# Optimization experiments

Hardware: AMD Instinct MI355X
Metric: run time of the kernel (lower is better)

## Reference

```python
import jax, jax.numpy as jnp
import numpy as np

V, E, H, C, T = 100000, 300, 512, 40, 4096  # vocab, embed, hidden, num_classes, seq_len


def setup_inputs() -> dict:
    key = jax.random.key(0)
    ks = jax.random.split(key, 19)
    s = lambda k, shape: jax.random.normal(k, shape, jnp.float32) * 0.05
    inp = {"x": jax.random.randint(ks[0], (T,), 0, V, dtype=jnp.int32)}
    inp["emb"] = s(ks[1], (V, E))  # frozen embedding table
    # PyTorch LSTM params, gate order (i, f, g, o); layer0 in=E, layer1 in=2H
    inp["Wih0f"] = s(ks[2], (4 * H, E)); inp["Whh0f"] = s(ks[3], (4 * H, H)); inp["b0f"] = s(ks[4], (4 * H,))
    inp["Wih0b"] = s(ks[5], (4 * H, E)); inp["Whh0b"] = s(ks[6], (4 * H, H)); inp["b0b"] = s(ks[7], (4 * H,))
    inp["Wih1f"] = s(ks[8], (4 * H, 2 * H)); inp["Whh1f"] = s(ks[9], (4 * H, H)); inp["b1f"] = s(ks[10], (4 * H,))
    inp["Wih1b"] = s(ks[11], (4 * H, 2 * H)); inp["Whh1b"] = s(ks[12], (4 * H, H)); inp["b1b"] = s(ks[13], (4 * H,))
    inp["Wc"] = s(ks[14], (C, 2 * H)); inp["bc"] = s(ks[15], (C,))
    inp["trans"] = s(ks[16], (C, C))  # CRF transitions prev->next
    inp["start"] = s(ks[17], (C,)); inp["end"] = s(ks[18], (C,))
    return inp


def _lstm_dir(x, Wih, Whh, b, reverse):
    # x: (T, D) unbatched; returns hidden states (T, H)
    Hd = Whh.shape[1]
    def step(carry, xt):
        h, c = carry
        g = xt @ Wih.T + h @ Whh.T + b  # (4H,)
        i, f, gg, o = jnp.split(g, 4)
        i = jax.nn.sigmoid(i); f = jax.nn.sigmoid(f)
        gg = jnp.tanh(gg); o = jax.nn.sigmoid(o)
        c = f * c + i * gg
        h = o * jnp.tanh(c)
        return (h, c), h
    xs = x[::-1] if reverse else x
    init = (jnp.zeros((Hd,), x.dtype), jnp.zeros((Hd,), x.dtype))
    _, hs = jax.lax.scan(step, init, xs)
    return hs[::-1] if reverse else hs


def _viterbi(emissions, trans, start, end):
    # emissions: (T, C); returns best path (T,) int32
    def fwd(score, em):
        m = score[:, None] + trans  # (C_prev, C_next)
        bp = jnp.argmax(m, axis=0).astype(jnp.int32)
        return jnp.max(m, axis=0) + em, bp
    score0 = start + emissions[0]
    final, bps = jax.lax.scan(fwd, score0, emissions[1:])  # bps: (T-1, C)
    last = jnp.argmax(final + end).astype(jnp.int32)
    def back(tag, bp):
        prev = bp[tag]
        return prev, prev
    _, path = jax.lax.scan(back, last, bps, reverse=True)  # tags 0..T-2 in order
    return jnp.concatenate([path, last[None]])


def reference(x, emb, Wih0f, Whh0f, b0f, Wih0b, Whh0b, b0b, Wih1f, Whh1f, b1f, Wih1b, Whh1b, b1b, Wc, bc, trans, start, end):
    e = emb[x]  # (T, E); dropout is identity at eval
    h0 = jnp.concatenate([_lstm_dir(e, Wih0f, Whh0f, b0f, False),
                          _lstm_dir(e, Wih0b, Whh0b, b0b, True)], axis=-1)  # (T, 2H)
    h1 = jnp.concatenate([_lstm_dir(h0, Wih1f, Whh1f, b1f, False),
                          _lstm_dir(h0, Wih1b, Whh1b, b1b, True)], axis=-1)  # (T, 2H)
    o = h1 @ Wc.T + bc  # (T, C)
    tag_scores = jax.nn.log_softmax(o, axis=1)
    tags = _viterbi(tag_scores, trans, start, end)
    return tag_scores, tags
```

## Files before the change

kernel.cpp:

```cpp
#include <hip/hip_runtime.h>


typedef unsigned int u32;
typedef unsigned long long u64;
typedef u32 u32x4 __attribute__((ext_vector_type(4)));

#define TT 4096
#define HH 512
#define CC 40
#define NG 2048

__device__ __forceinline__ float sigm(float x) { return 1.0f / (1.0f + __expf(-x)); }
__device__ __forceinline__ float tanh_(float x) { return 1.0f - 2.0f / (__expf(2.0f * x) + 1.0f); }

__device__ __forceinline__ void st_sys_u32(u32* p, u32 v) {
    asm volatile("global_store_dword %0, %1, off sc0 sc1"
                 :
                 : "v"(p), "v"(v)
                 : "memory");
}

__device__ __forceinline__ void ld_mall_b256(const float* p, u32x4& r0, u32x4& r1) {
    asm volatile(
        "global_load_dwordx4 %0, %2, off sc0 sc1\n\t"
        "global_load_dwordx4 %1, %2, off offset:16 sc0 sc1\n\t"
        "s_waitcnt vmcnt(0)"
        : "=&v"(r0), "=&v"(r1)
        : "v"(p)
        : "memory");
}

__global__ __launch_bounds__(256, 2) void gemm_f32_k(const float* __restrict__ A0,
                                                     const float* __restrict__ A1,
                                                     const int* __restrict__ xidx,
                                                     const float* __restrict__ W,
                                                     const float* __restrict__ bias,
                                                     float* __restrict__ C,
                                                     int M, int N, int K, int Ksplit) {
    __shared__ float sA[8][132];
    __shared__ float sW[8][132];
    int tid = threadIdx.x;
    int bn = blockIdx.x, bm = blockIdx.y;
    int tx = tid & 15, ty = tid >> 4;
    int srow = tid >> 1, skh = (tid & 1) * 4;

    int am = bm * 128 + srow;
    const float* arow0;
    const float* arow1 = nullptr;
    if (xidx) {
        arow0 = A0 + (size_t)xidx[am] * K;
    } else {
        arow0 = A0 + (size_t)am * Ksplit;
        arow1 = A1 + (size_t)am * Ksplit;
    }
    const float* wrow = W + (size_t)(bn * 128 + srow) * K;

    float acc[2][2][4][4] = {};

    for (int kc = 0; kc < K; kc += 8) {
        float4 av, wv;
        int k0 = kc + skh;
        if (kc + 8 <= K) {
            if (xidx || k0 + 4 <= Ksplit) av = *(const float4*)(arow0 + k0);
            else                          av = *(const float4*)(arow1 + (k0 - Ksplit));
            wv = *(const float4*)(wrow + k0);
        } else {
            float a_[4], w_[4];
#pragma unroll
            for (int j = 0; j < 4; j++) {
                int k = k0 + j;
                bool ok = k < K;
                a_[j] = ok ? ((xidx || k < Ksplit) ? arow0[k] : arow1[k - Ksplit]) : 0.f;
                w_[j] = ok ? wrow[k] : 0.f;
            }
            av = make_float4(a_[0], a_[1], a_[2], a_[3]);
            wv = make_float4(w_[0], w_[1], w_[2], w_[3]);
        }
        __syncthreads();
        sA[skh + 0][srow] = av.x; sA[skh + 1][srow] = av.y;
        sA[skh + 2][srow] = av.z; sA[skh + 3][srow] = av.w;
        sW[skh + 0][srow] = wv.x; sW[skh + 1][srow] = wv.y;
        sW[skh + 2][srow] = wv.z; sW[skh + 3][srow] = wv.w;
        __syncthreads();
#pragma unroll
        for (int k = 0; k < 8; k++) {
            float4 a0 = *(const float4*)&sA[k][ty * 4];
            float4 a1 = *(const float4*)&sA[k][64 + ty * 4];
            float4 w0 = *(const float4*)&sW[k][tx * 4];
            float4 w1 = *(const float4*)&sW[k][64 + tx * 4];
            float am_[2][4] = {{a0.x, a0.y, a0.z, a0.w}, {a1.x, a1.y, a1.z, a1.w}};
            float wn_[2][4] = {{w0.x, w0.y, w0.z, w0.w}, {w1.x, w1.y, w1.z, w1.w}};
#pragma unroll
            for (int p = 0; p < 2; p++)
#pragma unroll
                for (int q = 0; q < 2; q++)
#pragma unroll
                    for (int mi = 0; mi < 4; mi++)
#pragma unroll
                        for (int ni = 0; ni < 4; ni++)
                            acc[p][q][mi][ni] += am_[p][mi] * wn_[q][ni];
        }
    }

#pragma unroll
    for (int q = 0; q < 2; q++) {
        int gn = bn * 128 + q * 64 + tx * 4;
        float4 b4 = *(const float4*)&bias[gn];
#pragma unroll
        for (int p = 0; p < 2; p++) {
            int gm = bm * 128 + p * 64 + ty * 4;
#pragma unroll
            for (int mi = 0; mi < 4; mi++) {
                float4 o;
                o.x = acc[p][q][mi][0] + b4.x; o.y = acc[p][q][mi][1] + b4.y;
                o.z = acc[p][q][mi][2] + b4.z; o.w = acc[p][q][mi][3] + b4.w;
                *(float4*)&C[(size_t)(gm + mi) * N + gn] = o;
            }
        }
    }
}

__global__ __attribute__((amdgpu_flat_work_group_size(512, 512), amdgpu_waves_per_eu(2, 2)))
void lstm_phase_k(const float* __restrict__ WxF,
                  const float* __restrict__ WxB,
                  const float* __restrict__ WhhF,
                  const float* __restrict__ WhhB,
                  float* __restrict__ histF,
                  float* __restrict__ histB,
                  int phase) {
    const int wg = blockIdx.x & 31;
    const int dir = blockIdx.x >> 5;
    const int tid = threadIdx.x;
    const float* Wx = dir ? WxB : WxF;
    const float* Whh = dir ? WhhB : WhhF;
    float* hist = dir ? histB : histF;
    const u32 ENC = phase ? 0x7F800000u : 0u;

    const int r = tid >> 3, seg = tid & 7;
    const int grow = (r >> 4) * 512 + wg * 16 + (r & 15);

    float w[64];
    {
        const float* wr = Whh + (size_t)grow * HH + seg * 64;
#pragma unroll
        for (int i = 0; i < 16; i++) {
            float4 v = *(const float4*)(wr + i * 4);
            w[i * 4 + 0] = v.x; w[i * 4 + 1] = v.y; w[i * 4 + 2] = v.z; w[i * 4 + 3] = v.w;
        }
    }

    const int j = (tid < 62) ? (tid + (tid >= wg * 2 ? 2 : 0)) : 0;

    __shared__ float lds_h[8 * 68];
    __shared__ float lds_g[64];
    float c_state = 0.f;
    int capped = 0;

    for (int s = 0; s < TT; ++s) {
        const int t = dir ? (TT - 1 - s) : s;
        float wxv = 0.f;
        if (seg == 0) wxv = Wx[(size_t)t * NG + grow];

        if (s > 0) {
            const int tprev = dir ? (t + 1) : (t - 1);
            if (tid < 62) {
                const float* p = hist + (size_t)tprev * HH + j * 8;
                u32x4 v0, v1;
                if (!capped) {
                    int it = 0;
                    for (;;) {
                        ld_mall_b256(p, v0, v1);
                        bool ok;
                        if (phase) {
                            ok = ((v0.x & 0x7F800000u) >= 0x40000000u) &&
                                 ((v0.y & 0x7F800000u) >= 0x40000000u) &&
                                 ((v0.z & 0x7F800000u) >= 0x40000000u) &&
                                 ((v0.w & 0x7F800000u) >= 0x40000000u) &&
                                 ((v1.x & 0x7F800000u) >= 0x40000000u) &&
                                 ((v1.y & 0x7F800000u) >= 0x40000000u) &&
                                 ((v1.z & 0x7F800000u) >= 0x40000000u) &&
                                 ((v1.w & 0x7F800000u) >= 0x40000000u);
                        } else {
                            ok = (v0.x != 0xAAAAAAAAu) && (v0.y != 0xAAAAAAAAu) &&
                                 (v0.z != 0xAAAAAAAAu) && (v0.w != 0xAAAAAAAAu) &&
                                 (v1.x != 0xAAAAAAAAu) && (v1.y != 0xAAAAAAAAu) &&
                                 (v1.z != 0xAAAAAAAAu) && (v1.w != 0xAAAAAAAAu);
                        }
                        if (ok) break;
                        if (++it > (1 << 18)) { capped = 1; break; }
                    }
                } else {
                    ld_mall_b256(p, v0, v1);
                }
                float* dst = &lds_h[(j >> 3) * 68 + ((j & 7) * 8)];
                float4 f0, f1;
                f0.x = __uint_as_float(v0.x ^ ENC); f0.y = __uint_as_float(v0.y ^ ENC);
                f0.z = __uint_as_float(v0.z ^ ENC); f0.w = __uint_as_float(v0.w ^ ENC);
                f1.x = __uint_as_float(v1.x ^ ENC); f1.y = __uint_as_float(v1.y ^ ENC);
                f1.z = __uint_as_float(v1.z ^ ENC); f1.w = __uint_as_float(v1.w ^ ENC);
                *(float4*)dst = f0;
                *(float4*)(dst + 4) = f1;
            }
            __syncthreads();
            float a0 = 0.f, a1 = 0.f, a2 = 0.f, a3 = 0.f;
            const float4* hv4 = (const float4*)&lds_h[seg * 68];
#pragma unroll
            for (int i = 0; i < 16; i++) {
                float4 hv = hv4[i];
                a0 += w[i * 4 + 0] * hv.x;
                a1 += w[i * 4 + 1] * hv.y;
                a2 += w[i * 4 + 2] * hv.z;
                a3 += w[i * 4 + 3] * hv.w;
            }
            float acc = (a0 + a1) + (a2 + a3);
            acc += __shfl_xor(acc, 1);
            acc += __shfl_xor(acc, 2);
            acc += __shfl_xor(acc, 4);
            if (seg == 0) lds_g[r] = acc + wxv;
        } else {
            if (seg == 0) lds_g[r] = wxv;
        }
        __syncthreads();

        if (tid < 16) {
            float gi = lds_g[tid], gf = lds_g[16 + tid], gg = lds_g[32 + tid], go = lds_g[48 + tid];
            float iv = sigm(gi), fv = sigm(gf), gv = tanh_(gg), ov = sigm(go);
            c_state = fv * c_state + iv * gv;
            float h = ov * tanh_(c_state);
            int hidx = wg * 16 + tid;
            lds_h[(hidx >> 6) * 68 + (hidx & 63)] = h;
            st_sys_u32((u32*)&hist[(size_t)t * HH + hidx], __float_as_uint(h) ^ ENC);
        }
    }
}

__global__ __launch_bounds__(64, 4) void classifier_k(const float* __restrict__ histF,
                                                      const float* __restrict__ histB,
                                                      const float* __restrict__ Wc,
                                                      const float* __restrict__ bc,
                                                      float* __restrict__ outsc) {
    int t = blockIdx.x, lane = threadIdx.x;
    __shared__ float hrow[1024];
    const uint4* hf4 = (const uint4*)(histF + (size_t)t * HH);
    const uint4* hb4 = (const uint4*)(histB + (size_t)t * HH);
#pragma unroll
    for (int jj = 0; jj < 4; jj++) {
        int idx4 = jj * 64 + lane;
        uint4 u = (idx4 < 128) ? hf4[idx4] : hb4[idx4 - 128];
        u.x ^= 0x7F800000u; u.y ^= 0x7F800000u; u.z ^= 0x7F800000u; u.w ^= 0x7F800000u;
        float4 v;
        v.x = __uint_as_float(u.x); v.y = __uint_as_float(u.y);
        v.z = __uint_as_float(u.z); v.w = __uint_as_float(u.w);
        *(float4*)&hrow[idx4 * 4] = v;
    }
    __syncthreads();
    float o = 0.f;
    if (lane < CC) {
        o = bc[lane];
        const float4* wr = (const float4*)(Wc + (size_t)lane * 1024);
#pragma unroll 4
        for (int kk = 0; kk < 256; ++kk) {
            float4 w4 = wr[kk];
            float4 h4 = *(const float4*)&hrow[kk * 4];
            o += w4.x * h4.x + w4.y * h4.y + w4.z * h4.z + w4.w * h4.w;
        }
    }
    float m = (lane < CC) ? o : -1e30f;
#pragma unroll
    for (int d = 1; d < 64; d <<= 1) m = fmaxf(m, __shfl_xor(m, d));
    float ex = (lane < CC) ? __expf(o - m) : 0.f;
#pragma unroll
    for (int d = 1; d < 64; d <<= 1) ex += __shfl_xor(ex, d);
    float lse = m + __logf(ex);
    if (lane < CC) outsc[(size_t)t * CC + lane] = o - lse;
}

__global__ __launch_bounds__(64) void viterbi_k(const float* __restrict__ em,
                                               const float* __restrict__ trans,
                                               const float* __restrict__ startv,
                                               const float* __restrict__ endv,
                                               unsigned char* __restrict__ bp,
                                               float* __restrict__ outtags) {
    int lane = threadIdx.x;
    float tcol[CC];
#pragma unroll
    for (int p = 0; p < CC; p++) tcol[p] = 0.f;
    if (lane < CC) {
#pragma unroll
        for (int p = 0; p < CC; p++) tcol[p] = trans[p * CC + lane];
    }
    float s = (lane < CC) ? (startv[lane] + em[lane]) : 0.f;

    for (int t = 1; t < TT; ++t) {
        float emv = (lane < CC) ? em[(size_t)t * CC + lane] : 0.f;
        float b0 = -1e30f, b1 = -1e30f;
        int i0 = 0, i1 = 20;
#pragma unroll
        for (int p = 0; p < 20; p++) {
            float c0 = __shfl(s, p) + tcol[p];
            float c1 = __shfl(s, p + 20) + tcol[p + 20];
            if (c0 > b0) { b0 = c0; i0 = p; }
            if (c1 > b1) { b1 = c1; i1 = p + 20; }
        }
        float best = b0; int bi = i0;
        if (b1 > b0) { best = b1; bi = i1; }
        s = best + emv;
        if (lane < CC) bp[(size_t)t * CC + lane] = (unsigned char)bi;
    }
    float fv = (lane < CC) ? (s + endv[lane]) : -1e30f;
    int fi = (lane < CC) ? lane : 63;
#pragma unroll
    for (int d = 1; d < 64; d <<= 1) {
        float ov = __shfl_xor(fv, d);
        int oi = __shfl_xor(fi, d);
        if (ov > fv || (ov == fv && oi < fi)) { fv = ov; fi = oi; }
    }
    __threadfence();
    if (lane == 0) {
        int cur = fi;
        outtags[TT - 1] = (float)cur;
        for (int t = TT - 2; t >= 0; --t) {
            cur = bp[(size_t)(t + 1) * CC + cur];
            outtags[t] = (float)cur;
        }
    }
}

extern "C" void kernel_launch(void* const* d_in, const int* in_sizes, int n_in,
                              void* d_out, int out_size, void* d_ws, size_t ws_size,
                              hipStream_t stream) {
    const int*   x     = (const int*)d_in[0];
    const float* emb   = (const float*)d_in[1];
    const float* Wih0f = (const float*)d_in[2];
    const float* Whh0f = (const float*)d_in[3];
    const float* b0f   = (const float*)d_in[4];
    const float* Wih0b = (const float*)d_in[5];
    const float* Whh0b = (const float*)d_in[6];
    const float* b0b   = (const float*)d_in[7];
    const float* Wih1f = (const float*)d_in[8];
    const float* Whh1f = (const float*)d_in[9];
    const float* b1f   = (const float*)d_in[10];
    const float* Wih1b = (const float*)d_in[11];
    const float* Whh1b = (const float*)d_in[12];
    const float* b1b   = (const float*)d_in[13];
    const float* Wc    = (const float*)d_in[14];
    const float* bc    = (const float*)d_in[15];
    const float* trans = (const float*)d_in[16];
    const float* startv= (const float*)d_in[17];
    const float* endv  = (const float*)d_in[18];

    char* ws = (char*)d_ws;
    unsigned char* bp = (unsigned char*)(ws + 1024);
    float* WxF  = (float*)(ws + 262144);
    float* WxB  = (float*)(ws + 33816576);
    float* histF= (float*)(ws + 67371008);
    float* histB= (float*)(ws + 75759616);

    if (ws_size < (size_t)84148224) return;

    float* out_sc   = (float*)d_out;
    float* out_tags = out_sc + (size_t)TT * CC;

    gemm_f32_k<<<dim3(16, 32), 256, 0, stream>>>(emb, nullptr, x, Wih0f, b0f, WxF, TT, NG, 300, 300);
    gemm_f32_k<<<dim3(16, 32), 256, 0, stream>>>(emb, nullptr, x, Wih0b, b0b, WxB, TT, NG, 300, 300);
    lstm_phase_k<<<64, 512, 0, stream>>>(WxF, WxB, Whh0f, Whh0b, histF, histB, 0);
    gemm_f32_k<<<dim3(16, 32), 256, 0, stream>>>(histF, histB, nullptr, Wih1f, b1f, WxF, TT, NG, 1024, 512);
    gemm_f32_k<<<dim3(16, 32), 256, 0, stream>>>(histF, histB, nullptr, Wih1b, b1b, WxB, TT, NG, 1024, 512);
    lstm_phase_k<<<64, 512, 0, stream>>>(WxF, WxB, Whh1f, Whh1b, histF, histB, 1);
    classifier_k<<<TT, 64, 0, stream>>>(histF, histB, Wc, bc, out_sc);
    viterbi_k<<<1, 64, 0, stream>>>(out_sc, trans, startv, endv, bp, out_tags);
}
```

Baseline: 17.66 ms.

## Replace FP32 SIMT input-projection GEMMs with split-bf16 MFMA GEMMs

The four input-projection GEMMs move from a scalar FP32 outer-product kernel to a matrix-core kernel. Each FP32 operand is split into bf16 hi and lo parts, and three bf16 MFMAs (hi*hi, hi*lo, lo*hi) are accumulated to get close to FP32 accuracy. Operands are staged in XOR-swizzled LDS tiles with a K tile of 32. The goal is to cut the GEMM part of total time, but the sequential LSTM recurrence probably dominates, so the end-to-end effect may be small, and there is a slight precision risk.

```diff
diff --git a/kernel.cpp b/kernel.cpp
--- a/kernel.cpp
+++ b/kernel.cpp
@@ -4,6 +4,8 @@
 typedef unsigned int u32;
 typedef unsigned long long u64;
 typedef u32 u32x4 __attribute__((ext_vector_type(4)));
+typedef __attribute__((ext_vector_type(8))) short s16x8;
+typedef __attribute__((ext_vector_type(4))) float f32x4;
 
 #define TT 4096
 #define HH 512
@@ -30,92 +32,121 @@
         : "memory");
 }
 
-__global__ __launch_bounds__(256, 2) void gemm_f32_k(const float* __restrict__ A0,
-                                                     const float* __restrict__ A1,
-                                                     const int* __restrict__ xidx,
-                                                     const float* __restrict__ W,
-                                                     const float* __restrict__ bias,
-                                                     float* __restrict__ C,
-                                                     int M, int N, int K, int Ksplit) {
-    __shared__ float sA[8][132];
-    __shared__ float sW[8][132];
-    int tid = threadIdx.x;
-    int bn = blockIdx.x, bm = blockIdx.y;
-    int tx = tid & 15, ty = tid >> 4;
-    int srow = tid >> 1, skh = (tid & 1) * 4;
-
-    int am = bm * 128 + srow;
-    const float* arow0;
-    const float* arow1 = nullptr;
-    if (xidx) {
-        arow0 = A0 + (size_t)xidx[am] * K;
-    } else {
-        arow0 = A0 + (size_t)am * Ksplit;
-        arow1 = A1 + (size_t)am * Ksplit;
-    }
+__device__ __forceinline__ void split_pack8(const float* f, s16x8& hi, s16x8& lo) {
+#pragma unroll
+    for (int j = 0; j < 8; j++) {
+        float x = f[j];
+        u32 h = __float_as_uint(x) & 0xFFFF0000u;
+        float hf = __uint_as_float(h);
+        hi[j] = (short)(h >> 16);
+        lo[j] = (short)(__float_as_uint(x - hf) >> 16);
+    }
+}
+
+__global__ __launch_bounds__(256, 2) void gemm_bf16s_k(const float* __restrict__ A0,
+                                                       const float* __restrict__ A1,
+                                                       const int* __restrict__ xidx,
+                                                       const float* __restrict__ W,
+                                                       const float* __restrict__ bias,
+                                                       float* __restrict__ C,
+                                                       int M, int N, int K, int Ksplit) {
+    __shared__ __align__(16) short sAh[128 * 32];
+    __shared__ __align__(16) short sAl[128 * 32];
+    __shared__ __align__(16) short sWh[128 * 32];
+    __shared__ __align__(16) short sWl[128 * 32];
+    const int tid = threadIdx.x;
+    const int bn = blockIdx.x, bm = blockIdx.y;
+    const int wid = tid >> 6, lane = tid & 63;
+    const int qm = (wid >> 1) * 64, qn = (wid & 1) * 64;
+    const int fr = lane & 15, fq = lane >> 4;
+
+    const int srow = tid >> 1;
+    const int kh = (tid & 1) * 16;
+
+    const int am = bm * 128 + srow;
+    const float* arow = xidx ? (A0 + (size_t)xidx[am] * K) : nullptr;
+    const float* a0r = xidx ? nullptr : (A0 + (size_t)am * Ksplit);
+    const float* a1r = xidx ? nullptr : (A1 + (size_t)am * Ksplit);
     const float* wrow = W + (size_t)(bn * 128 + srow) * K;
 
-    float acc[2][2][4][4] = {};
-
-    for (int kc = 0; kc < K; kc += 8) {
-        float4 av, wv;
-        int k0 = kc + skh;
-        if (kc + 8 <= K) {
-            if (xidx || k0 + 4 <= Ksplit) av = *(const float4*)(arow0 + k0);
-            else                          av = *(const float4*)(arow1 + (k0 - Ksplit));
-            wv = *(const float4*)(wrow + k0);
+    f32x4 acc[4][4] = {};
+
+    const int NP = (K + 31) >> 5;
+    for (int kp = 0; kp < NP; kp++) {
+        const int kb = kp * 32 + kh;
+        float fa[16], fw[16];
+        if (kb + 16 <= K) {
+#pragma unroll
+            for (int j = 0; j < 16; j += 4) {
+                int k = kb + j;
+                const float* s = xidx ? (arow + k)
+                                      : ((k < Ksplit) ? (a0r + k) : (a1r + (k - Ksplit)));
+                float4 v = *(const float4*)s;
+                fa[j] = v.x; fa[j + 1] = v.y; fa[j + 2] = v.z; fa[j + 3] = v.w;
+                float4 wv = *(const float4*)(wrow + k);
+                fw[j] = wv.x; fw[j + 1] = wv.y; fw[j + 2] = wv.z; fw[j + 3] = wv.w;
+            }
         } else {
-            float a_[4], w_[4];
-#pragma unroll
-            for (int j = 0; j < 4; j++) {
-                int k = k0 + j;
-                bool ok = k < K;
-                a_[j] = ok ? ((xidx || k < Ksplit) ? arow0[k] : arow1[k - Ksplit]) : 0.f;
-                w_[j] = ok ? wrow[k] : 0.f;
+#pragma unroll
+            for (int j = 0; j < 16; j++) {
+                int k = kb + j;
+                float av = 0.f, wv = 0.f;
+                if (k < K) {
+                    av = xidx ? arow[k] : ((k < Ksplit) ? a0r[k] : a1r[k - Ksplit]);
+                    wv = wrow[k];
+                }
+                fa[j] = av; fw[j] = wv;
             }
-            av = make_float4(a_[0], a_[1], a_[2], a_[3]);
-            wv = make_float4(w_[0], w_[1], w_[2], w_[3]);
         }
         __syncthreads();
-        sA[skh + 0][srow] = av.x; sA[skh + 1][srow] = av.y;
-        sA[skh + 2][srow] = av.z; sA[skh + 3][srow] = av.w;
-        sW[skh + 0][srow] = wv.x; sW[skh + 1][srow] = wv.y;
-        sW[skh + 2][srow] = wv.z; sW[skh + 3][srow] = wv.w;
+#pragma unroll
+        for (int c = 0; c < 2; c++) {
+            int ch = (tid & 1) * 2 + c;
+            int pch = ch ^ ((srow >> 1) & 3);
+            int off = srow * 32 + pch * 8;
+            s16x8 hi, lo;
+            split_pack8(fa + c * 8, hi, lo);
+            *(s16x8*)&sAh[off] = hi;
+            *(s16x8*)&sAl[off] = lo;
+            split_pack8(fw + c * 8, hi, lo);
+            *(s16x8*)&sWh[off] = hi;
+            *(s16x8*)&sWl[off] = lo;
+        }
         __syncthreads();
-#pragma unroll
-        for (int k = 0; k < 8; k++) {
-            float4 a0 = *(const float4*)&sA[k][ty * 4];
-            float4 a1 = *(const float4*)&sA[k][64 + ty * 4];
-            float4 w0 = *(const float4*)&sW[k][tx * 4];
-            float4 w1 = *(const float4*)&sW[k][64 + tx * 4];
-            float am_[2][4] = {{a0.x, a0.y, a0.z, a0.w}, {a1.x, a1.y, a1.z, a1.w}};
-            float wn_[2][4] = {{w0.x, w0.y, w0.z, w0.w}, {w1.x, w1.y, w1.z, w1.w}};
-#pragma unroll
-            for (int p = 0; p < 2; p++)
-#pragma unroll
-                for (int q = 0; q < 2; q++)
-#pragma unroll
-                    for (int mi = 0; mi < 4; mi++)
-#pragma unroll
-                        for (int ni = 0; ni < 4; ni++)
-                            acc[p][q][mi][ni] += am_[p][mi] * wn_[q][ni];
-        }
-    }
-
-#pragma unroll
-    for (int q = 0; q < 2; q++) {
-        int gn = bn * 128 + q * 64 + tx * 4;
-        float4 b4 = *(const float4*)&bias[gn];
-#pragma unroll
-        for (int p = 0; p < 2; p++) {
-            int gm = bm * 128 + p * 64 + ty * 4;
-#pragma unroll
-            for (int mi = 0; mi < 4; mi++) {
-                float4 o;
-                o.x = acc[p][q][mi][0] + b4.x; o.y = acc[p][q][mi][1] + b4.y;
-                o.z = acc[p][q][mi][2] + b4.z; o.w = acc[p][q][mi][3] + b4.w;
-                *(float4*)&C[(size_t)(gm + mi) * N + gn] = o;
+
+        s16x8 ah[4], al[4];
+#pragma unroll
+        for (int m = 0; m < 4; m++) {
+            int row = qm + m * 16 + fr;
+            int off = row * 32 + ((fq ^ ((row >> 1) & 3)) * 8);
+            ah[m] = *(const s16x8*)&sAh[off];
+            al[m] = *(const s16x8*)&sAl[off];
+        }
+#pragma unroll
+        for (int n = 0; n < 4; n++) {
+            int row = qn + n * 16 + fr;
+            int off = row * 32 + ((fq ^ ((row >> 1) & 3)) * 8);
+            s16x8 bh = *(const s16x8*)&sWh[off];
+            s16x8 bl = *(const s16x8*)&sWl[off];
+#pragma unroll
+            for (int m = 0; m < 4; m++) {
+                acc[m][n] = __builtin_amdgcn_mfma_f32_16x16x32_bf16(ah[m], bh, acc[m][n], 0, 0, 0);
+                acc[m][n] = __builtin_amdgcn_mfma_f32_16x16x32_bf16(ah[m], bl, acc[m][n], 0, 0, 0);
+                acc[m][n] = __builtin_amdgcn_mfma_f32_16x16x32_bf16(al[m], bh, acc[m][n], 0, 0, 0);
             }
+        }
+    }
+
+#pragma unroll
+    for (int n = 0; n < 4; n++) {
+        int gcol = bn * 128 + qn + n * 16 + fr;
+        float b = bias[gcol];
+#pragma unroll
+        for (int m = 0; m < 4; m++) {
+            int rbase = bm * 128 + qm + m * 16 + fq * 4;
+#pragma unroll
+            for (int r2 = 0; r2 < 4; r2++)
+                C[(size_t)(rbase + r2) * N + gcol] = acc[m][n][r2] + b;
         }
     }
 }
@@ -361,11 +392,11 @@
     float* out_sc   = (float*)d_out;
     float* out_tags = out_sc + (size_t)TT * CC;
 
-    gemm_f32_k<<<dim3(16, 32), 256, 0, stream>>>(emb, nullptr, x, Wih0f, b0f, WxF, TT, NG, 300, 300);
-    gemm_f32_k<<<dim3(16, 32), 256, 0, stream>>>(emb, nullptr, x, Wih0b, b0b, WxB, TT, NG, 300, 300);
+    gemm_bf16s_k<<<dim3(16, 32), 256, 0, stream>>>(emb, nullptr, x, Wih0f, b0f, WxF, TT, NG, 300, 300);
+    gemm_bf16s_k<<<dim3(16, 32), 256, 0, stream>>>(emb, nullptr, x, Wih0b, b0b, WxB, TT, NG, 300, 300);
     lstm_phase_k<<<64, 512, 0, stream>>>(WxF, WxB, Whh0f, Whh0b, histF, histB, 0);
-    gemm_f32_k<<<dim3(16, 32), 256, 0, stream>>>(histF, histB, nullptr, Wih1f, b1f, WxF, TT, NG, 1024, 512);
-    gemm_f32_k<<<dim3(16, 32), 256, 0, stream>>>(histF, histB, nullptr, Wih1b, b1b, WxB, TT, NG, 1024, 512);
+    gemm_bf16s_k<<<dim3(16, 32), 256, 0, stream>>>(histF, histB, nullptr, Wih1f, b1f, WxF, TT, NG, 1024, 512);
+    gemm_bf16s_k<<<dim3(16, 32), 256, 0, stream>>>(histF, histB, nullptr, Wih1b, b1b, WxB, TT, NG, 1024, 512);
     lstm_phase_k<<<64, 512, 0, stream>>>(WxF, WxB, Whh1f, Whh1b, histF, histB, 1);
     classifier_k<<<TT, 64, 0, stream>>>(histF, histB, Wc, bc, out_sc);
     viterbi_k<<<1, 64, 0, stream>>>(out_sc, trans, startv, endv, bp, out_tags);
```

Result: faster. 17.29 ms (-2.1%).
